# Performance work log

Measured on AMD Instinct MI355X. Metric: run time of the kernel, lower is better.

## Reference

```python
import jax, jax.numpy as jnp
import numpy as np

N_NODES = 50000
N_EDGES = 800000
NFEAT, NHID, NCLASS = 512, 256, 128
N_UV = 2048


def gcn_layer(x, adj_row, adj_col, adj_val, W, b):
    # support = x @ W ; out = A @ support (sparse COO spmm) + b
    support = x @ W                                   # [N, out]
    msgs = adj_val[:, None] * support[adj_col]        # [E, out]
    out = jax.ops.segment_sum(msgs, adj_row, num_segments=N_NODES)
    return out + b


def setup_inputs() -> dict:
    key = jax.random.key(0)
    ks = jax.random.split(key, 12)
    u = jax.random.randint(ks[0], (N_UV,), 0, N_NODES)
    v = jax.random.randint(ks[1], (N_UV,), 0, N_NODES)
    x = jax.random.normal(ks[2], (N_NODES, NFEAT), dtype=jnp.float32)
    adj_row = jnp.sort(jax.random.randint(ks[3], (N_EDGES,), 0, N_NODES))
    adj_col = jax.random.randint(ks[4], (N_EDGES,), 0, N_NODES)
    adj_val = jax.random.uniform(ks[5], (N_EDGES,), dtype=jnp.float32)
    s1 = 1.0 / np.sqrt(NHID)
    s2 = 1.0 / np.sqrt(NCLASS)
    W1 = jax.random.uniform(ks[6], (NFEAT, NHID), minval=-s1, maxval=s1, dtype=jnp.float32)
    b1 = jax.random.uniform(ks[7], (NHID,), minval=-s1, maxval=s1, dtype=jnp.float32)
    W2 = jax.random.uniform(ks[8], (NHID, NCLASS), minval=-s2, maxval=s2, dtype=jnp.float32)
    b2 = jax.random.uniform(ks[9], (NCLASS,), minval=-s2, maxval=s2, dtype=jnp.float32)
    We = jax.random.normal(ks[10], (NCLASS, NCLASS), dtype=jnp.float32) * (1.0 / np.sqrt(NCLASS))
    return {"u": u, "v": v, "x": x, "adj_row": adj_row, "adj_col": adj_col,
            "adj_val": adj_val, "W1": W1, "b1": b1, "W2": W2, "b2": b2, "We": We}


def reference(u, v, x, adj_row, adj_col, adj_val, W1, b1, W2, b2, We):
    # layer 1: GCN + ReLU (dropout is identity in eval mode)
    h = jax.nn.relu(gcn_layer(x, adj_row, adj_col, adj_val, W1, b1))
    # layer 2: GCN
    z = gcn_layer(h, adj_row, adj_col, adj_val, W2, b2)          # [N, nclass]
    # edge scoring: sigmoid(w_edge(z[u]) @ z[v].T)
    zu = z[u] @ We.T                                             # [U, nclass] (nn.Linear: x @ W.T)
    zv = z[v]                                                    # [V, nclass]
    p_uv = jax.nn.sigmoid(zu @ zv.T)                             # [U, V]
    return p_uv
```

## Files before the change

kernel.cpp:

```cpp
#include <hip/hip_runtime.h>
#include <hip/hip_bf16.h>
#include <math.h>

#define N_NODES 50000
#define N_EDGES 800000
#define NFEAT   512
#define NHID    256
#define NCLASS  128
#define N_UV    2048

#define Q24_SCALE  524288.0f
#define Q24_INV    1.9073486328125e-6f

typedef __bf16    bf16x8 __attribute__((ext_vector_type(8)));
typedef short     s16x8  __attribute__((ext_vector_type(8)));
typedef float     f32x4  __attribute__((ext_vector_type(4)));

struct __attribute__((packed)) U3 { unsigned a, b, c; };

__device__ __forceinline__ unsigned short bf16_rn(float f) {
  unsigned u = __float_as_uint(f);
  u += 0x7fffu + ((u >> 16) & 1u);
  return (unsigned short)(u >> 16);
}
__device__ __forceinline__ float bf16_to_f(unsigned short h) {
  return __uint_as_float(((unsigned)h) << 16);
}
__device__ __forceinline__ void unpack24(unsigned a, unsigned b, unsigned c,
                                         int& e0, int& e1, int& e2, int& e3) {
  e0 = ((int)(a << 8)) >> 8;
  e1 = ((int)((b << 16) | ((a >> 24) << 8))) >> 8;
  e2 = ((int)((c << 24) | ((b >> 16) << 8))) >> 8;
  e3 = ((int)c) >> 8;
}

#define LDSPAD 72

template <bool ASPLIT, int OMODE>
__global__ __launch_bounds__(256, 4) void gemm_mfma_wide(
    const float* __restrict__ Af,
    const unsigned short* __restrict__ Ahi, const unsigned short* __restrict__ Alo,
    const unsigned short* __restrict__ BThi, const unsigned short* __restrict__ BTlo,
    const unsigned short* __restrict__ BThi2, const unsigned short* __restrict__ BTlo2,
    float* __restrict__ C, unsigned char* __restrict__ Cq,
    unsigned short* __restrict__ Chi, unsigned short* __restrict__ Clo,
    const float* __restrict__ bias, const float* __restrict__ bias2,
    int M, int N, int K) {
  __shared__ unsigned short sAh[2][64 * LDSPAD];
  __shared__ unsigned short sAl[2][64 * LDSPAD];

  const int tid  = threadIdx.x;
  const int lane = tid & 63;
  const int wave = tid >> 6;
  const int wn   = wave << 5;
  const int lm   = lane & 15;
  const int quad = lane >> 4;
  const int m0   = blockIdx.y * 64;
  const int n0   = blockIdx.x * 128;

  const bool vh = (OMODE == 5) && ((int)blockIdx.y >= (M >> 7));
  const unsigned short* selBh = (OMODE == 5 && vh) ? BThi2 : BThi;
  const unsigned short* selBl = (OMODE == 5 && vh) ? BTlo2 : BTlo;
  const float*          selBi = (OMODE == 5 && vh) ? bias2 : bias;

  const int r32 = tid >> 4;
  const int c32 = (tid & 15) * 4;
  const int r16 = tid >> 3;
  const int c16 = (tid & 7) * 8;

  float4 pA[4]; s16x8 pAh[2], pAl[2];

  f32x4 acc[4][2];
#pragma unroll
  for (int i = 0; i < 4; ++i)
#pragma unroll
    for (int j = 0; j < 2; ++j)
#pragma unroll
      for (int r = 0; r < 4; ++r) acc[i][j][r] = 0.f;

#define LOAD_TILE(k0)                                                          \
  do {                                                                         \
    if (ASPLIT) {                                                              \
      _Pragma("unroll") for (int p = 0; p < 4; ++p) {                          \
        const int m = m0 + p * 16 + r32;                                       \
        pA[p] = make_float4(0.f, 0.f, 0.f, 0.f);                               \
        if (m < M) pA[p] = *(const float4*)&Af[(size_t)m * K + (k0) + c32];    \
      }                                                                        \
    } else {                                                                   \
      _Pragma("unroll") for (int p = 0; p < 2; ++p) {                          \
        const int m = m0 + p * 32 + r16;                                       \
        _Pragma("unroll") for (int e = 0; e < 8; ++e) { pAh[p][e] = 0; pAl[p][e] = 0; } \
        if (m < M) {                                                           \
          pAh[p] = *(const s16x8*)&Ahi[(size_t)m * K + (k0) + c16];            \
          pAl[p] = *(const s16x8*)&Alo[(size_t)m * K + (k0) + c16];            \
        }                                                                      \
      }                                                                        \
    }                                                                          \
  } while (0)

#define SPLIT4W(v, hv, lv)                                                     \
  hv.x = bf16_rn(v.x); lv.x = bf16_rn(v.x - bf16_to_f(hv.x));                  \
  hv.y = bf16_rn(v.y); lv.y = bf16_rn(v.y - bf16_to_f(hv.y));                  \
  hv.z = bf16_rn(v.z); lv.z = bf16_rn(v.z - bf16_to_f(hv.z));                  \
  hv.w = bf16_rn(v.w); lv.w = bf16_rn(v.w - bf16_to_f(hv.w));

#define STORE_TILE(buf)                                                        \
  do {                                                                         \
    if (ASPLIT) {                                                              \
      _Pragma("unroll") for (int p = 0; p < 4; ++p) {                          \
        ushort4 hv, lv; SPLIT4W(pA[p], hv, lv);                                \
        const int row = p * 16 + r32;                                          \
        *(ushort4*)&sAh[buf][row * LDSPAD + c32] = hv;                         \
        *(ushort4*)&sAl[buf][row * LDSPAD + c32] = lv;                         \
      }                                                                        \
    } else {                                                                   \
      _Pragma("unroll") for (int p = 0; p < 2; ++p) {                          \
        const int row = p * 32 + r16;                                          \
        *(s16x8*)&sAh[buf][row * LDSPAD + c16] = pAh[p];                       \
        *(s16x8*)&sAl[buf][row * LDSPAD + c16] = pAl[p];                       \
      }                                                                        \
    }                                                                          \
  } while (0)

  LOAD_TILE(0);
  STORE_TILE(0);

  const unsigned short* Bhrow = selBh + (size_t)(n0 + wn + lm) * K;
  const unsigned short* Blrow = selBl + (size_t)(n0 + wn + lm) * K;

  __syncthreads();

  const int NT = K >> 6;
  for (int t = 0; t < NT; ++t) {
    const int k0  = t << 6;
    const int cur = t & 1;
    const unsigned short* bufh = &sAh[cur][0];
    const unsigned short* bufl = &sAl[cur][0];

    bf16x8 bH[2][2], bL[2][2];
#pragma unroll
    for (int ks = 0; ks < 2; ++ks)
#pragma unroll
      for (int j = 0; j < 2; ++j) {
        const size_t off = (size_t)(j * 16) * K + k0 + ks * 32 + quad * 8;
        bH[ks][j] = __builtin_bit_cast(bf16x8, *(const s16x8*)(Bhrow + off));
        bL[ks][j] = __builtin_bit_cast(bf16x8, *(const s16x8*)(Blrow + off));
      }

    if (t + 1 < NT) LOAD_TILE(k0 + 64);

#pragma unroll
    for (int ks = 0; ks < 2; ++ks) {
      const int koff = ks * 32 + quad * 8;
#pragma unroll
      for (int i = 0; i < 4; ++i) {
        const int r = i * 16 + lm;
        const bf16x8 aH = __builtin_bit_cast(bf16x8, *(const s16x8*)&bufh[r * LDSPAD + koff]);
        const bf16x8 aL = __builtin_bit_cast(bf16x8, *(const s16x8*)&bufl[r * LDSPAD + koff]);
#pragma unroll
        for (int j = 0; j < 2; ++j) {
          acc[i][j] = __builtin_amdgcn_mfma_f32_16x16x32_bf16(aH, bH[ks][j], acc[i][j], 0, 0, 0);
          acc[i][j] = __builtin_amdgcn_mfma_f32_16x16x32_bf16(aH, bL[ks][j], acc[i][j], 0, 0, 0);
          acc[i][j] = __builtin_amdgcn_mfma_f32_16x16x32_bf16(aL, bH[ks][j], acc[i][j], 0, 0, 0);
        }
      }
    }

    if (t + 1 < NT) STORE_TILE(cur ^ 1);
    __syncthreads();
  }

#pragma unroll
  for (int i = 0; i < 4; ++i)
#pragma unroll
    for (int j = 0; j < 2; ++j) {
      const int col = n0 + wn + j * 16 + lm;
      const float bb = (OMODE == 3 || OMODE == 5) ? selBi[col] : 0.f;
#pragma unroll
      for (int r = 0; r < 4; ++r) {
        const int row = m0 + i * 16 + quad * 4 + r;
        if (row < M) {
          float v = acc[i][j][r];
          if (OMODE == 2) {
            int q = __float2int_rn(v * Q24_SCALE);
            q = q > 8388607 ? 8388607 : (q < -8388608 ? -8388608 : q);
            unsigned char* p = Cq + ((size_t)row * N + col) * 3;
            p[0] = (unsigned char)(q & 0xFF);
            p[1] = (unsigned char)((q >> 8) & 0xFF);
            p[2] = (unsigned char)((q >> 16) & 0xFF);
          } else if (OMODE == 1) {
            C[(size_t)row * N + col] = 1.f / (1.f + expf(-v));
          } else if (OMODE == 3) {
            C[(size_t)row * N + col] = v + bb;
          } else if (OMODE == 5) {
            v += bb;
            if (!vh) {
              C[(size_t)row * N + col] = v;
            } else {
              const unsigned short h = bf16_rn(v);
              const size_t o = (size_t)(row - (M >> 1)) * N + col;
              Chi[o] = h;
              Clo[o] = bf16_rn(v - bf16_to_f(h));
            }
          } else {
            C[(size_t)row * N + col] = v;
          }
        }
      }
    }
#undef LOAD_TILE
#undef STORE_TILE
#undef SPLIT4W
}

__global__ __launch_bounds__(256) void prep_all(
    const int* __restrict__ rows, int* __restrict__ row_ptr,
    const float* __restrict__ W1, unsigned short* __restrict__ W1Thi,
    unsigned short* __restrict__ W1Tlo,
    const float* __restrict__ W2, unsigned short* __restrict__ W2Thi,
    unsigned short* __restrict__ W2Tlo) {
  const int idx = blockIdx.x * 256 + threadIdx.x;
  if (idx < N_EDGES) {
    const int r = rows[idx];
    const int rprev = (idx == 0) ? -1 : rows[idx - 1];
    for (int n = rprev + 1; n <= r; ++n) row_ptr[n] = idx;
    if (idx == N_EDGES - 1)
      for (int n = r + 1; n <= N_NODES; ++n) row_ptr[n] = N_EDGES;
  }
  if (idx < NFEAT * NHID) {
    const int n = idx / NFEAT;
    const int k = idx - n * NFEAT;
    const float f = W1[(size_t)k * NHID + n];
    const unsigned short h = bf16_rn(f);
    W1Thi[idx] = h;
    W1Tlo[idx] = bf16_rn(f - bf16_to_f(h));
  }
  if (idx < NHID * NCLASS) {
    const int n = idx / NHID;
    const int k = idx - n * NHID;
    const float f = W2[(size_t)k * NCLASS + n];
    const unsigned short h = bf16_rn(f);
    W2Thi[idx] = h;
    W2Tlo[idx] = bf16_rn(f - bf16_to_f(h));
  }
}

__global__ __launch_bounds__(256) void prep_w2e(
    const float* __restrict__ W2, const float* __restrict__ We,
    const float* __restrict__ b2,
    unsigned short* __restrict__ W2eThi, unsigned short* __restrict__ W2eTlo,
    float* __restrict__ b2e) {
  const int idx = blockIdx.x * 256 + threadIdx.x;
  const int n = idx >> 8;
  const int k = idx & 255;
  const float4* wr = (const float4*)(We + (size_t)n * NCLASS);
  const float4* ar = (const float4*)(W2 + (size_t)k * NCLASS);
  float s = 0.f;
#pragma unroll
  for (int c = 0; c < NCLASS / 4; ++c) {
    const float4 a = ar[c], w = wr[c];
    s = fmaf(a.x, w.x, s); s = fmaf(a.y, w.y, s);
    s = fmaf(a.z, w.z, s); s = fmaf(a.w, w.w, s);
  }
  const unsigned short h = bf16_rn(s);
  W2eThi[idx] = h;
  W2eTlo[idx] = bf16_rn(s - bf16_to_f(h));
  if (idx < NCLASS) {
    const float4* br = (const float4*)b2;
    const float4* w2 = (const float4*)(We + (size_t)idx * NCLASS);
    float t = 0.f;
#pragma unroll
    for (int c = 0; c < NCLASS / 4; ++c) {
      const float4 a = br[c], w = w2[c];
      t = fmaf(a.x, w.x, t); t = fmaf(a.y, w.y, t);
      t = fmaf(a.z, w.z, t); t = fmaf(a.w, w.w, t);
    }
    b2e[idx] = t;
  }
}

__global__ __launch_bounds__(256, 4) void spmm256_q24_f32(
    const unsigned char* __restrict__ Sq, const int* __restrict__ row_ptr,
    const int* __restrict__ cols, const float* __restrict__ vals,
    const float4* __restrict__ bias4, float4* __restrict__ outF) {
  const int wave = threadIdx.x >> 6;
  const int lane = threadIdx.x & 63;
  const int node = blockIdx.x * 4 + wave;

  const int lou = __builtin_amdgcn_readfirstlane(row_ptr[node]);
  const int hiu = __builtin_amdgcn_readfirstlane(row_ptr[node + 1]);

  float4 acc = make_float4(0.f, 0.f, 0.f, 0.f);
  const int lane12 = lane * 12;

  for (int base = lou; base < hiu; base += 16) {
    int   c[16];
    float w[16];
    if (base + 16 <= hiu) {
#pragma unroll
      for (int t = 0; t < 16; ++t) {
        c[t] = cols[base + t];
        w[t] = vals[base + t] * Q24_INV;
      }
    } else {
#pragma unroll
      for (int t = 0; t < 16; ++t) {
        const int idx = base + t;
        const int ide = idx < hiu ? idx : hiu - 1;
        c[t] = cols[ide];
        w[t] = idx < hiu ? vals[ide] * Q24_INV : 0.f;
      }
    }
    U3 d[16];
#pragma unroll
    for (int t = 0; t < 16; ++t)
      d[t] = *(const U3*)&Sq[(size_t)c[t] * (NHID * 3) + lane12];
#pragma unroll
    for (int t = 0; t < 16; ++t) {
      int e0, e1, e2, e3;
      unpack24(d[t].a, d[t].b, d[t].c, e0, e1, e2, e3);
      acc.x = fmaf(w[t], (float)e0, acc.x);
      acc.y = fmaf(w[t], (float)e1, acc.y);
      acc.z = fmaf(w[t], (float)e2, acc.z);
      acc.w = fmaf(w[t], (float)e3, acc.w);
    }
  }

  const float4 b = bias4[lane];
  acc.x = fmaxf(acc.x + b.x, 0.f);
  acc.y = fmaxf(acc.y + b.y, 0.f);
  acc.z = fmaxf(acc.z + b.z, 0.f);
  acc.w = fmaxf(acc.w + b.w, 0.f);

  outF[(size_t)node * 64 + lane] = acc;
}

__global__ __launch_bounds__(256, 4) void spmm256_f32_list(
    const float4* __restrict__ H4, const int* __restrict__ row_ptr,
    const int* __restrict__ cols, const float* __restrict__ vals,
    const int* __restrict__ u, const int* __restrict__ v,
    float4* __restrict__ out4) {
  const int wave = threadIdx.x >> 6;
  const int lane = threadIdx.x & 63;
  const int idx  = blockIdx.x * 4 + wave;
  const int node = idx < N_UV ? u[idx] : v[idx - N_UV];

  const int lou = __builtin_amdgcn_readfirstlane(row_ptr[node]);
  const int hiu = __builtin_amdgcn_readfirstlane(row_ptr[node + 1]);

  float4 acc = make_float4(0.f, 0.f, 0.f, 0.f);

  for (int base = lou; base < hiu; base += 16) {
    int   c[16];
    float w[16];
    if (base + 16 <= hiu) {
#pragma unroll
      for (int t = 0; t < 16; ++t) { c[t] = cols[base + t]; w[t] = vals[base + t]; }
    } else {
#pragma unroll
      for (int t = 0; t < 16; ++t) {
        const int e = base + t;
        const int ie = e < hiu ? e : hiu - 1;
        c[t] = cols[ie];
        w[t] = e < hiu ? vals[ie] : 0.f;
      }
    }
    float4 r[16];
#pragma unroll
    for (int t = 0; t < 16; ++t) r[t] = H4[(size_t)c[t] * 64 + lane];
#pragma unroll
    for (int t = 0; t < 16; ++t) {
      acc.x = fmaf(w[t], r[t].x, acc.x); acc.y = fmaf(w[t], r[t].y, acc.y);
      acc.z = fmaf(w[t], r[t].z, acc.z); acc.w = fmaf(w[t], r[t].w, acc.w);
    }
  }

  out4[(size_t)idx * 64 + lane] = acc;
}

extern "C" void kernel_launch(void* const* d_in, const int* in_sizes, int n_in,
                              void* d_out, int out_size, void* d_ws, size_t ws_size,
                              hipStream_t stream) {
  const int*   u       = (const int*)  d_in[0];
  const int*   v       = (const int*)  d_in[1];
  const float* x       = (const float*)d_in[2];
  const int*   adj_row = (const int*)  d_in[3];
  const int*   adj_col = (const int*)  d_in[4];
  const float* adj_val = (const float*)d_in[5];
  const float* W1      = (const float*)d_in[6];
  const float* b1      = (const float*)d_in[7];
  const float* W2      = (const float*)d_in[8];
  const float* b2      = (const float*)d_in[9];
  const float* We      = (const float*)d_in[10];
  float* out = (float*)d_out;

  char* wsb = (char*)d_ws;
  unsigned char* S1q = (unsigned char*)wsb;
  float* ZUV2 = (float*)wsb;
  float* ZU   = (float*)(wsb + (4u << 20));
  unsigned short* ZVhi = (unsigned short*)(wsb + (5u << 20));
  unsigned short* ZVlo = (unsigned short*)(wsb + (5u << 20) + (512u << 10));
  float* Hf = (float*)(wsb + (size_t)N_NODES * NHID * sizeof(float));
  unsigned short* W1Thi = (unsigned short*)out;
  unsigned short* W1Tlo = W1Thi + NHID * NFEAT;
  unsigned short* W2Thi = W1Tlo + NHID * NFEAT;
  unsigned short* W2Tlo = W2Thi + NCLASS * NHID;
  int* row_ptr = (int*)(W2Tlo + NCLASS * NHID);
  unsigned short* W2eThi = (unsigned short*)(row_ptr + N_NODES + 4);
  unsigned short* W2eTlo = W2eThi + NCLASS * NHID;
  float* b2e = (float*)(W2eTlo + NCLASS * NHID);

  prep_all<<<(N_EDGES + 255) / 256, 256, 0, stream>>>(
      adj_row, row_ptr, W1, W1Thi, W1Tlo, W2, W2Thi, W2Tlo);
  prep_w2e<<<(NCLASS * NHID) / 256, 256, 0, stream>>>(
      W2, We, b2, W2eThi, W2eTlo, b2e);

  gemm_mfma_wide<true, 2>
      <<<dim3(NHID / 128, (N_NODES + 63) / 64), 256, 0, stream>>>(
      x, nullptr, nullptr, W1Thi, W1Tlo, nullptr, nullptr,
      nullptr, S1q, nullptr, nullptr, nullptr, nullptr, N_NODES, NHID, NFEAT);

  spmm256_q24_f32<<<N_NODES / 4, 256, 0, stream>>>(
      S1q, row_ptr, adj_col, adj_val, (const float4*)b1, (float4*)Hf);

  spmm256_f32_list<<<(2 * N_UV) / 4, 256, 0, stream>>>(
      (const float4*)Hf, row_ptr, adj_col, adj_val, u, v, (float4*)ZUV2);

  gemm_mfma_wide<true, 5>
      <<<dim3(NCLASS / 128, (2 * N_UV) / 64), 256, 0, stream>>>(
      ZUV2, nullptr, nullptr, W2eThi, W2eTlo, W2Thi, W2Tlo,
      ZU, nullptr, ZVhi, ZVlo, b2e, b2, 2 * N_UV, NCLASS, NHID);

  gemm_mfma_wide<true, 1>
      <<<dim3(N_UV / 128, N_UV / 64), 256, 0, stream>>>(
      ZU, nullptr, nullptr, ZVhi, ZVlo, nullptr, nullptr,
      out, nullptr, nullptr, nullptr, nullptr, nullptr, N_UV, N_UV, NCLASS);
}
```

Before: 364.6 us.

## Single-buffer LDS A tile and raise GEMM launch bounds to 8 waves per SIMD

The GEMM kernel drops LDS double buffering for the A tile and uses one buffer with two barriers per K step: store, sync, compute, then sync before the next store. Launch bounds rise from 4 to 8 blocks per CU, which halves LDS per block and pushes the compiler toward fewer registers so more blocks can be resident. The aim is to hide latency through occupancy rather than software pipelining. In exchange it adds a barrier per iteration, loses the overlap of the LDS store with compute, and may cause register spills under the tighter register budget.

```diff
diff --git a/kernel.cpp b/kernel.cpp
--- a/kernel.cpp
+++ b/kernel.cpp
@@ -37,7 +37,7 @@
 #define LDSPAD 72
 
 template <bool ASPLIT, int OMODE>
-__global__ __launch_bounds__(256, 4) void gemm_mfma_wide(
+__global__ __launch_bounds__(256, 8) void gemm_mfma_wide(
     const float* __restrict__ Af,
     const unsigned short* __restrict__ Ahi, const unsigned short* __restrict__ Alo,
     const unsigned short* __restrict__ BThi, const unsigned short* __restrict__ BTlo,
@@ -46,8 +46,8 @@
     unsigned short* __restrict__ Chi, unsigned short* __restrict__ Clo,
     const float* __restrict__ bias, const float* __restrict__ bias2,
     int M, int N, int K) {
-  __shared__ unsigned short sAh[2][64 * LDSPAD];
-  __shared__ unsigned short sAl[2][64 * LDSPAD];
+  __shared__ unsigned short sAh[64 * LDSPAD];
+  __shared__ unsigned short sAl[64 * LDSPAD];
 
   const int tid  = threadIdx.x;
   const int lane = tid & 63;
@@ -104,38 +104,33 @@
   hv.z = bf16_rn(v.z); lv.z = bf16_rn(v.z - bf16_to_f(hv.z));                  \
   hv.w = bf16_rn(v.w); lv.w = bf16_rn(v.w - bf16_to_f(hv.w));
 
-#define STORE_TILE(buf)                                                        \
+#define STORE_TILE()                                                           \
   do {                                                                         \
     if (ASPLIT) {                                                              \
       _Pragma("unroll") for (int p = 0; p < 4; ++p) {                          \
         ushort4 hv, lv; SPLIT4W(pA[p], hv, lv);                                \
         const int row = p * 16 + r32;                                          \
-        *(ushort4*)&sAh[buf][row * LDSPAD + c32] = hv;                         \
-        *(ushort4*)&sAl[buf][row * LDSPAD + c32] = lv;                         \
+        *(ushort4*)&sAh[row * LDSPAD + c32] = hv;                              \
+        *(ushort4*)&sAl[row * LDSPAD + c32] = lv;                              \
       }                                                                        \
     } else {                                                                   \
       _Pragma("unroll") for (int p = 0; p < 2; ++p) {                          \
         const int row = p * 32 + r16;                                          \
-        *(s16x8*)&sAh[buf][row * LDSPAD + c16] = pAh[p];                       \
-        *(s16x8*)&sAl[buf][row * LDSPAD + c16] = pAl[p];                       \
+        *(s16x8*)&sAh[row * LDSPAD + c16] = pAh[p];                            \
+        *(s16x8*)&sAl[row * LDSPAD + c16] = pAl[p];                            \
       }                                                                        \
     }                                                                          \
   } while (0)
 
   LOAD_TILE(0);
-  STORE_TILE(0);
 
   const unsigned short* Bhrow = selBh + (size_t)(n0 + wn + lm) * K;
   const unsigned short* Blrow = selBl + (size_t)(n0 + wn + lm) * K;
 
-  __syncthreads();
-
-  const int NT = K >> 6;
-  for (int t = 0; t < NT; ++t) {
-    const int k0  = t << 6;
-    const int cur = t & 1;
-    const unsigned short* bufh = &sAh[cur][0];
-    const unsigned short* bufl = &sAl[cur][0];
+  for (int k0 = 0; k0 < K; k0 += 64) {
+    if (k0) __syncthreads();
+    STORE_TILE();
+    __syncthreads();
 
     bf16x8 bH[2][2], bL[2][2];
 #pragma unroll
@@ -147,7 +142,7 @@
         bL[ks][j] = __builtin_bit_cast(bf16x8, *(const s16x8*)(Blrow + off));
       }
 
-    if (t + 1 < NT) LOAD_TILE(k0 + 64);
+    if (k0 + 64 < K) LOAD_TILE(k0 + 64);
 
 #pragma unroll
     for (int ks = 0; ks < 2; ++ks) {
@@ -155,8 +150,8 @@
 #pragma unroll
       for (int i = 0; i < 4; ++i) {
         const int r = i * 16 + lm;
-        const bf16x8 aH = __builtin_bit_cast(bf16x8, *(const s16x8*)&bufh[r * LDSPAD + koff]);
-        const bf16x8 aL = __builtin_bit_cast(bf16x8, *(const s16x8*)&bufl[r * LDSPAD + koff]);
+        const bf16x8 aH = __builtin_bit_cast(bf16x8, *(const s16x8*)&sAh[r * LDSPAD + koff]);
+        const bf16x8 aL = __builtin_bit_cast(bf16x8, *(const s16x8*)&sAl[r * LDSPAD + koff]);
 #pragma unroll
         for (int j = 0; j < 2; ++j) {
           acc[i][j] = __builtin_amdgcn_mfma_f32_16x16x32_bf16(aH, bH[ks][j], acc[i][j], 0, 0, 0);
@@ -165,9 +160,6 @@
         }
       }
     }
-
-    if (t + 1 < NT) STORE_TILE(cur ^ 1);
-    __syncthreads();
   }
 
 #pragma unroll
```

After: 685.5 us. 1.88x slower.
